# Optimization experiments

Hardware: AMD Instinct MI355X
Metric: run time of the kernel (lower is better)

Reference implementation:

```python
import jax, jax.numpy as jnp
import numpy as np

EMBED = 2048
HEADS = 16
KV_LEN = 4096
HEAD_DIM = EMBED // HEADS
LN_EPS = 1e-6


def _layernorm(x, scale, bias):
    m = jnp.mean(x, axis=-1, keepdims=True)
    v = jnp.var(x, axis=-1, keepdims=True)
    return (x - m) / jnp.sqrt(v + LN_EPS) * scale + bias


def setup_inputs() -> dict:
    key = jax.random.key(0)
    ks = jax.random.split(key, 12)
    d = EMBED
    s = 1.0 / np.sqrt(d)

    def W(k):
        return jax.random.normal(k, (d, d), jnp.float32) * s

    return {
        "x": jax.random.normal(ks[0], (d,), jnp.float32),
        "cache1": jax.random.normal(ks[1], (KV_LEN, HEADS, HEAD_DIM), jnp.float32),
        "cache2": jax.random.normal(ks[2], (KV_LEN, HEADS, HEAD_DIM), jnp.float32),
        "Wv": W(ks[3]), "bv": jnp.zeros((d,), jnp.float32),
        "Wq": W(ks[4]), "bq": jnp.zeros((d,), jnp.float32),
        "Wk": W(ks[5]), "bk": jnp.zeros((d,), jnp.float32),
        "Wo": W(ks[6]), "bo": jnp.zeros((d,), jnp.float32),
        "W1": W(ks[7]), "b1": jnp.zeros((d,), jnp.float32),
        "W2": W(ks[8]), "b2": jnp.zeros((d,), jnp.float32),
        "ln1_s": jnp.ones((d,), jnp.float32), "ln1_b": jnp.zeros((d,), jnp.float32),
        "ln2_s": jnp.ones((d,), jnp.float32), "ln2_b": jnp.zeros((d,), jnp.float32),
    }


def reference(x, cache1, cache2, Wv, bv, Wq, bq, Wk, bk, Wo, bo,
              W1, b1, W2, b2, ln1_s, ln1_b, ln2_s, ln2_b):
    H, hd = HEADS, HEAD_DIM
    # QKV projections for the single query token
    v_i = (x @ Wv + bv).reshape(1, H, hd)
    q_i = (x @ Wq + bq).reshape(H, hd)
    k_i = (x @ Wk + bk).reshape(1, H, hd)
    # roll caches: drop oldest, append newest
    v = jnp.concatenate((cache1[1:], v_i), axis=0)  # [K, H, hd]
    k = jnp.concatenate((cache2[1:], k_i), axis=0)
    # valid positions: any nonzero value in the v cache slot
    mask = jnp.any(v != 0, axis=(1, 2))  # [K]
    att = jnp.einsum('hd,khd->hk', q_i, k) / jnp.sqrt(jnp.float32(hd))
    att = jnp.where(mask, att, -jnp.inf)
    att = jax.nn.softmax(att, axis=-1)
    values = jnp.einsum('hk,khd->hd', att, v).reshape(EMBED)
    out = values @ Wo + bo
    # residual + LN, FFN (dropout deterministic -> no-op), residual + LN
    x1 = _layernorm(x + out, ln1_s, ln1_b)
    h = jax.nn.relu(x1 @ W1 + b1) @ W2 + b2
    x2 = _layernorm(x1 + h, ln2_s, ln2_b)
    return (x2, v, k)
```

## Files before the change

### kernel.cpp

```cpp
#include <hip/hip_runtime.h>
#include <hip/hip_bf16.h>
#include <stdint.h>

#define D    2048
#define H    16
#define HD   128
#define KV   4096
#define NCH  64
#define RPC  (D / NCH)
#define AVCH 64
#define AVR  (KV / AVCH)
#define RSQRT_HD 0.08838834764831845f

typedef __attribute__((ext_vector_type(4))) float floatx4;


__global__ void k_matvec_part(const float* __restrict__ W0,
                              const float* __restrict__ W1p,
                              const float* __restrict__ W2p,
                              const float* __restrict__ xin,
                              float* __restrict__ part) {
    const float* W = (blockIdx.y == 0) ? W0 : (blockIdx.y == 1 ? W1p : W2p);
    int c0 = threadIdx.x * 4;
    int r0 = blockIdx.x * RPC;
    floatx4 a0 = {0.f, 0.f, 0.f, 0.f};
    floatx4 a1 = {0.f, 0.f, 0.f, 0.f};
    for (int r = r0; r < r0 + RPC; ++r) {
        float xv = xin[r];
        floatx4 w0 = *reinterpret_cast<const floatx4*>(W + (size_t)r * D + c0);
        floatx4 w1 = *reinterpret_cast<const floatx4*>(W + (size_t)r * D + c0 + 1024);
        a0 += xv * w0;
        a1 += xv * w1;
    }
    float* p = part + ((size_t)blockIdx.y * NCH + blockIdx.x) * D;
    *reinterpret_cast<floatx4*>(p + c0) = a0;
    *reinterpret_cast<floatx4*>(p + c0 + 1024) = a1;
}

__global__ void k_qkv_reduce(const float* __restrict__ part,
                             const float* __restrict__ bq,
                             const float* __restrict__ bk,
                             const float* __restrict__ bv,
                             float* __restrict__ q, float* __restrict__ kn,
                             float* __restrict__ vn) {
    int t = blockIdx.x * 256 + threadIdx.x;
    int m = t >> 11;
    int col = t & (D - 1);
    float s = 0.f;
    const float* p = part + (size_t)m * NCH * D + col;
    for (int c = 0; c < NCH; ++c) s += p[(size_t)c * D];
    if (m == 0)      q[col]  = s + bq[col];
    else if (m == 1) kn[col] = s + bk[col];
    else             vn[col] = s + bv[col];
}

__global__ void k_roll_logits(const float* __restrict__ cache1,
                              const float* __restrict__ cache2,
                              const float* __restrict__ q,
                              const float* __restrict__ kn,
                              const float* __restrict__ vn,
                              float* __restrict__ outv,
                              float* __restrict__ outk,
                              float* __restrict__ att) {
    int wave = threadIdx.x >> 6;
    int lane = threadIdx.x & 63;
    int kk = blockIdx.x * 4 + wave;
    float pc[8];
    bool nz = false;

    if (kk < KV - 1) {
        const float* vsrc = cache1 + (size_t)(kk + 1) * D;
        const float* ksrc = cache2 + (size_t)(kk + 1) * D;
        float* vdst = outv + (size_t)kk * D;
        float* kdst = outk + (size_t)kk * D;
#pragma unroll
        for (int c = 0; c < 8; ++c) {
            int e = c * 256 + lane * 4;
            floatx4 v4 = *reinterpret_cast<const floatx4*>(vsrc + e);
            *reinterpret_cast<floatx4*>(vdst + e) = v4;
            nz = nz | (v4[0] != 0.f) | (v4[1] != 0.f) | (v4[2] != 0.f) | (v4[3] != 0.f);
            floatx4 k4 = *reinterpret_cast<const floatx4*>(ksrc + e);
            *reinterpret_cast<floatx4*>(kdst + e) = k4;
            floatx4 q4 = *reinterpret_cast<const floatx4*>(q + e);
            pc[c] = q4[0]*k4[0] + q4[1]*k4[1] + q4[2]*k4[2] + q4[3]*k4[3];
        }
    } else {
        float* vdst = outv + (size_t)kk * D;
        float* kdst = outk + (size_t)kk * D;
#pragma unroll
        for (int c = 0; c < 8; ++c) {
            int e = c * 256 + lane * 4;
            floatx4 v4, k4;
#pragma unroll
            for (int j = 0; j < 4; ++j) {
                v4[j] = vn[e + j];
                k4[j] = kn[e + j];
            }
            *reinterpret_cast<floatx4*>(vdst + e) = v4;
            *reinterpret_cast<floatx4*>(kdst + e) = k4;
            nz = nz | (v4[0] != 0.f) | (v4[1] != 0.f) | (v4[2] != 0.f) | (v4[3] != 0.f);
            floatx4 q4 = *reinterpret_cast<const floatx4*>(q + e);
            pc[c] = q4[0]*k4[0] + q4[1]*k4[1] + q4[2]*k4[2] + q4[3]*k4[3];
        }
    }

    unsigned long long bal = __ballot(nz ? 1 : 0);
    bool anynz = (bal != 0ULL);

#pragma unroll
    for (int c = 0; c < 8; ++c) {
        float v = pc[c];
        v += __shfl_xor(v, 1);
        v += __shfl_xor(v, 2);
        v += __shfl_xor(v, 4);
        v += __shfl_xor(v, 8);
        v += __shfl_xor(v, 16);
        pc[c] = v;
    }
    if ((lane & 31) == 0) {
        int hi = lane >> 5;
#pragma unroll
        for (int c = 0; c < 8; ++c) {
            int h = c * 2 + hi;
            att[(size_t)h * KV + kk] = anynz ? pc[c] * RSQRT_HD : -INFINITY;
        }
    }
}

__global__ void k_softmax(float* __restrict__ att) {
    __shared__ float sred[4];
    int h = blockIdx.x;
    float* a = att + (size_t)h * KV;
    int t = threadIdx.x;
    float v[16];
    float m = -INFINITY;
#pragma unroll
    for (int i = 0; i < 16; ++i) {
        v[i] = a[i * 256 + t];
        m = fmaxf(m, v[i]);
    }
    for (int s = 32; s >= 1; s >>= 1) m = fmaxf(m, __shfl_xor(m, s));
    if ((t & 63) == 0) sred[t >> 6] = m;
    __syncthreads();
    m = fmaxf(fmaxf(sred[0], sred[1]), fmaxf(sred[2], sred[3]));
    __syncthreads();
    float sum = 0.f;
#pragma unroll
    for (int i = 0; i < 16; ++i) {
        v[i] = __expf(v[i] - m);
        sum += v[i];
    }
    for (int s = 32; s >= 1; s >>= 1) sum += __shfl_xor(sum, s);
    if ((t & 63) == 0) sred[t >> 6] = sum;
    __syncthreads();
    sum = sred[0] + sred[1] + sred[2] + sred[3];
    float inv = 1.0f / sum;
#pragma unroll
    for (int i = 0; i < 16; ++i) a[i * 256 + t] = v[i] * inv;
}

__global__ void k_av_part(const float* __restrict__ outv,
                          const float* __restrict__ att,
                          float* __restrict__ pav) {
    int h = blockIdx.y;
    int c = blockIdx.x;
    int lane = threadIdx.x;
    int dg = (lane & 31) * 4;
    int ks = lane >> 5;
    floatx4 acc = {0.f, 0.f, 0.f, 0.f};
    int kk0 = c * AVR;
    for (int i = 0; i < AVR / 2; ++i) {
        int kk = kk0 + i * 2 + ks;
        float a = att[(size_t)h * KV + kk];
        floatx4 v4 = *reinterpret_cast<const floatx4*>(outv + (size_t)kk * D + h * HD + dg);
        acc += a * v4;
    }
#pragma unroll
    for (int j = 0; j < 4; ++j) acc[j] += __shfl_xor(acc[j], 32);
    if (lane < 32) {
        *reinterpret_cast<floatx4*>(pav + (size_t)c * D + h * HD + dg) = acc;
    }
}

__global__ void k_av_reduce(const float* __restrict__ pav, float* __restrict__ values) {
    int e = blockIdx.x * 256 + threadIdx.x;
    float s = 0.f;
    for (int c = 0; c < AVCH; ++c) s += pav[(size_t)c * D + e];
    values[e] = s;
}

__global__ void k_mv_reduce(const float* __restrict__ part,
                            const float* __restrict__ bias,
                            float* __restrict__ out, int relu) {
    int col = blockIdx.x * 256 + threadIdx.x;
    float s = 0.f;
    for (int c = 0; c < NCH; ++c) s += part[(size_t)c * D + col];
    s += bias[col];
    if (relu) s = fmaxf(s, 0.0f);
    out[col] = s;
}

__global__ void k_ln(const float* __restrict__ a, const float* __restrict__ b,
                     const float* __restrict__ sc, const float* __restrict__ bi,
                     float* __restrict__ out) {
    __shared__ float sred[4];
    int t = threadIdx.x;
    float loc[8];
    float s = 0.f;
#pragma unroll
    for (int i = 0; i < 8; ++i) {
        int e = i * 256 + t;
        float v = a[e] + b[e];
        loc[i] = v;
        s += v;
    }
    for (int m = 32; m >= 1; m >>= 1) s += __shfl_xor(s, m);
    if ((t & 63) == 0) sred[t >> 6] = s;
    __syncthreads();
    float mean = (sred[0] + sred[1] + sred[2] + sred[3]) * (1.0f / D);
    __syncthreads();
    float vs = 0.f;
#pragma unroll
    for (int i = 0; i < 8; ++i) {
        float d = loc[i] - mean;
        vs += d * d;
    }
    for (int m = 32; m >= 1; m >>= 1) vs += __shfl_xor(vs, m);
    if ((t & 63) == 0) sred[t >> 6] = vs;
    __syncthreads();
    float var = (sred[0] + sred[1] + sred[2] + sred[3]) * (1.0f / D);
    float inv = 1.0f / sqrtf(var + 1e-6f);
#pragma unroll
    for (int i = 0; i < 8; ++i) {
        int e = i * 256 + t;
        out[e] = (loc[i] - mean) * inv * sc[e] + bi[e];
    }
}

extern "C" void kernel_launch(void* const* d_in, const int* in_sizes, int n_in,
                              void* d_out, int out_size, void* d_ws, size_t ws_size,
                              hipStream_t stream) {
    const float* x      = (const float*)d_in[0];
    const float* cache1 = (const float*)d_in[1];
    const float* cache2 = (const float*)d_in[2];
    const float* Wv     = (const float*)d_in[3];
    const float* bv     = (const float*)d_in[4];
    const float* Wq     = (const float*)d_in[5];
    const float* bq     = (const float*)d_in[6];
    const float* Wk     = (const float*)d_in[7];
    const float* bk     = (const float*)d_in[8];
    const float* Wo     = (const float*)d_in[9];
    const float* bo     = (const float*)d_in[10];
    const float* W1     = (const float*)d_in[11];
    const float* b1     = (const float*)d_in[12];
    const float* W2     = (const float*)d_in[13];
    const float* b2     = (const float*)d_in[14];
    const float* l1s    = (const float*)d_in[15];
    const float* l1b    = (const float*)d_in[16];
    const float* l2s    = (const float*)d_in[17];
    const float* l2b    = (const float*)d_in[18];

    float* out   = (float*)d_out;
    float* outx2 = out;
    float* outv  = out + D;
    float* outk  = out + D + (size_t)KV * D;

    float* w      = (float*)d_ws;
    float* q      = w + 2048;
    float* kn     = w + 4096;
    float* vn     = w + 6144;
    float* att    = w + 8192;
    float* values = w + 73728;
    float* aout   = w + 75776;
    float* x1     = w + 77824;
    float* h1     = w + 79872;
    float* h2     = w + 81920;
    float* part   = w + 83968;
    float* pav    = w + 477184;

    k_matvec_part<<<dim3(NCH, 3), 256, 0, stream>>>(Wq, Wk, Wv, x, part);
    k_qkv_reduce<<<24, 256, 0, stream>>>(part, bq, bk, bv, q, kn, vn);
    k_roll_logits<<<KV / 4, 256, 0, stream>>>(cache1, cache2, q, kn, vn, outv, outk, att);
    k_softmax<<<H, 256, 0, stream>>>(att);
    k_av_part<<<dim3(AVCH, H), 64, 0, stream>>>(outv, att, pav);
    k_av_reduce<<<8, 256, 0, stream>>>(pav, values);
    k_matvec_part<<<dim3(NCH, 1), 256, 0, stream>>>(Wo, Wo, Wo, values, part);
    k_mv_reduce<<<8, 256, 0, stream>>>(part, bo, aout, 0);
    k_ln<<<1, 256, 0, stream>>>(x, aout, l1s, l1b, x1);
    k_matvec_part<<<dim3(NCH, 1), 256, 0, stream>>>(W1, W1, W1, x1, part);
    k_mv_reduce<<<8, 256, 0, stream>>>(part, b1, h1, 1);
    k_matvec_part<<<dim3(NCH, 1), 256, 0, stream>>>(W2, W2, W2, h1, part);
    k_mv_reduce<<<8, 256, 0, stream>>>(part, b2, h2, 0);
    k_ln<<<1, 256, 0, stream>>>(x1, h2, l2s, l2b, outx2);
}
```

Measured before the change: 281.5 us.

## Replace split-K partial buffers and reduce kernels with atomic accumulation and fused biases

Matvec and attention-value kernels now accumulate straight into zeroed outputs with float atomics, so the separate partial-sum reduce kernels and their scratch traffic go away. Biases and the ReLU are folded into the consumers (roll_logits, layernorm, the next matvec's input load), and a memset zeroes the accumulators up front. The matvec also loads 16 rows of weights at a time for more memory-level parallelism. This cuts the kernel launch count, at the cost of atomic contention and nondeterministic summation order.

After: 292.4 us. +3.9%, slower.

```diff
diff --git a/kernel.cpp b/kernel.cpp
--- a/kernel.cpp
+++ b/kernel.cpp
@@ -6,59 +6,46 @@
 #define H    16
 #define HD   128
 #define KV   4096
-#define NCH  64
-#define RPC  (D / NCH)
-#define AVCH 64
-#define AVR  (KV / AVCH)
 #define RSQRT_HD 0.08838834764831845f
 
 typedef __attribute__((ext_vector_type(4))) float floatx4;
 
 
-__global__ void k_matvec_part(const float* __restrict__ W0,
-                              const float* __restrict__ W1p,
-                              const float* __restrict__ W2p,
-                              const float* __restrict__ xin,
-                              float* __restrict__ part) {
-    const float* W = (blockIdx.y == 0) ? W0 : (blockIdx.y == 1 ? W1p : W2p);
+__global__ void k_matvec(const float* __restrict__ Wa, const float* __restrict__ Wb,
+                         const float* __restrict__ Wc, const float* __restrict__ xin,
+                         const float* __restrict__ prebias,
+                         float* __restrict__ dst) {
+    const float* W = (blockIdx.y == 0) ? Wa : (blockIdx.y == 1 ? Wb : Wc);
+    float* d = dst + (size_t)blockIdx.y * D;
     int c0 = threadIdx.x * 4;
-    int r0 = blockIdx.x * RPC;
-    floatx4 a0 = {0.f, 0.f, 0.f, 0.f};
-    floatx4 a1 = {0.f, 0.f, 0.f, 0.f};
-    for (int r = r0; r < r0 + RPC; ++r) {
-        float xv = xin[r];
-        floatx4 w0 = *reinterpret_cast<const floatx4*>(W + (size_t)r * D + c0);
-        floatx4 w1 = *reinterpret_cast<const floatx4*>(W + (size_t)r * D + c0 + 1024);
-        a0 += xv * w0;
-        a1 += xv * w1;
-    }
-    float* p = part + ((size_t)blockIdx.y * NCH + blockIdx.x) * D;
-    *reinterpret_cast<floatx4*>(p + c0) = a0;
-    *reinterpret_cast<floatx4*>(p + c0 + 1024) = a1;
-}
-
-__global__ void k_qkv_reduce(const float* __restrict__ part,
-                             const float* __restrict__ bq,
-                             const float* __restrict__ bk,
-                             const float* __restrict__ bv,
-                             float* __restrict__ q, float* __restrict__ kn,
-                             float* __restrict__ vn) {
-    int t = blockIdx.x * 256 + threadIdx.x;
-    int m = t >> 11;
-    int col = t & (D - 1);
-    float s = 0.f;
-    const float* p = part + (size_t)m * NCH * D + col;
-    for (int c = 0; c < NCH; ++c) s += p[(size_t)c * D];
-    if (m == 0)      q[col]  = s + bq[col];
-    else if (m == 1) kn[col] = s + bk[col];
-    else             vn[col] = s + bv[col];
+    int r0 = blockIdx.x * 32;
+    floatx4 acc = {0.f, 0.f, 0.f, 0.f};
+    for (int rb = 0; rb < 2; ++rb) {
+        const float* Wp = W + (size_t)(r0 + rb * 16) * D + c0;
+        floatx4 w[16];
+#pragma unroll
+        for (int i = 0; i < 16; ++i)
+            w[i] = *reinterpret_cast<const floatx4*>(Wp + (size_t)i * D);
+#pragma unroll
+        for (int i = 0; i < 16; ++i) {
+            int r = r0 + rb * 16 + i;
+            float t = xin[r];
+            if (prebias) t = fmaxf(t + prebias[r], 0.f);
+            acc += t * w[i];
+        }
+    }
+    atomicAdd(&d[c0 + 0], acc[0]);
+    atomicAdd(&d[c0 + 1], acc[1]);
+    atomicAdd(&d[c0 + 2], acc[2]);
+    atomicAdd(&d[c0 + 3], acc[3]);
 }
 
 __global__ void k_roll_logits(const float* __restrict__ cache1,
                               const float* __restrict__ cache2,
-                              const float* __restrict__ q,
-                              const float* __restrict__ kn,
-                              const float* __restrict__ vn,
+                              const float* __restrict__ qs,
+                              const float* __restrict__ bq,
+                              const float* __restrict__ bk,
+                              const float* __restrict__ bv,
                               float* __restrict__ outv,
                               float* __restrict__ outk,
                               float* __restrict__ att) {
@@ -67,39 +54,43 @@
     int kk = blockIdx.x * 4 + wave;
     float pc[8];
     bool nz = false;
+    float* vdst = outv + (size_t)kk * D;
+    float* kdst = outk + (size_t)kk * D;
 
     if (kk < KV - 1) {
         const float* vsrc = cache1 + (size_t)(kk + 1) * D;
         const float* ksrc = cache2 + (size_t)(kk + 1) * D;
-        float* vdst = outv + (size_t)kk * D;
-        float* kdst = outk + (size_t)kk * D;
+        floatx4 v[8], k[8];
+#pragma unroll
+        for (int c = 0; c < 8; ++c)
+            v[c] = *reinterpret_cast<const floatx4*>(vsrc + c * 256 + lane * 4);
+#pragma unroll
+        for (int c = 0; c < 8; ++c)
+            k[c] = *reinterpret_cast<const floatx4*>(ksrc + c * 256 + lane * 4);
 #pragma unroll
         for (int c = 0; c < 8; ++c) {
             int e = c * 256 + lane * 4;
-            floatx4 v4 = *reinterpret_cast<const floatx4*>(vsrc + e);
-            *reinterpret_cast<floatx4*>(vdst + e) = v4;
-            nz = nz | (v4[0] != 0.f) | (v4[1] != 0.f) | (v4[2] != 0.f) | (v4[3] != 0.f);
-            floatx4 k4 = *reinterpret_cast<const floatx4*>(ksrc + e);
-            *reinterpret_cast<floatx4*>(kdst + e) = k4;
-            floatx4 q4 = *reinterpret_cast<const floatx4*>(q + e);
-            pc[c] = q4[0]*k4[0] + q4[1]*k4[1] + q4[2]*k4[2] + q4[3]*k4[3];
+            *reinterpret_cast<floatx4*>(vdst + e) = v[c];
+            *reinterpret_cast<floatx4*>(kdst + e) = k[c];
+            nz = nz | (v[c][0] != 0.f) | (v[c][1] != 0.f) | (v[c][2] != 0.f) | (v[c][3] != 0.f);
+            floatx4 q4 = *reinterpret_cast<const floatx4*>(qs + e);
+            floatx4 b4 = *reinterpret_cast<const floatx4*>(bq + e);
+            q4 += b4;
+            pc[c] = q4[0]*k[c][0] + q4[1]*k[c][1] + q4[2]*k[c][2] + q4[3]*k[c][3];
         }
     } else {
-        float* vdst = outv + (size_t)kk * D;
-        float* kdst = outk + (size_t)kk * D;
 #pragma unroll
         for (int c = 0; c < 8; ++c) {
             int e = c * 256 + lane * 4;
-            floatx4 v4, k4;
-#pragma unroll
-            for (int j = 0; j < 4; ++j) {
-                v4[j] = vn[e + j];
-                k4[j] = kn[e + j];
-            }
+            floatx4 v4 = *reinterpret_cast<const floatx4*>(qs + 2 * D + e);
+            floatx4 k4 = *reinterpret_cast<const floatx4*>(qs + D + e);
+            v4 += *reinterpret_cast<const floatx4*>(bv + e);
+            k4 += *reinterpret_cast<const floatx4*>(bk + e);
             *reinterpret_cast<floatx4*>(vdst + e) = v4;
             *reinterpret_cast<floatx4*>(kdst + e) = k4;
             nz = nz | (v4[0] != 0.f) | (v4[1] != 0.f) | (v4[2] != 0.f) | (v4[3] != 0.f);
-            floatx4 q4 = *reinterpret_cast<const floatx4*>(q + e);
+            floatx4 q4 = *reinterpret_cast<const floatx4*>(qs + e);
+            q4 += *reinterpret_cast<const floatx4*>(bq + e);
             pc[c] = q4[0]*k4[0] + q4[1]*k4[1] + q4[2]*k4[2] + q4[3]*k4[3];
         }
     }
@@ -159,17 +150,18 @@
     for (int i = 0; i < 16; ++i) a[i * 256 + t] = v[i] * inv;
 }
 
-__global__ void k_av_part(const float* __restrict__ outv,
-                          const float* __restrict__ att,
-                          float* __restrict__ pav) {
+__global__ void k_av(const float* __restrict__ outv,
+                     const float* __restrict__ att,
+                     float* __restrict__ values) {
     int h = blockIdx.y;
     int c = blockIdx.x;
     int lane = threadIdx.x;
     int dg = (lane & 31) * 4;
     int ks = lane >> 5;
     floatx4 acc = {0.f, 0.f, 0.f, 0.f};
-    int kk0 = c * AVR;
-    for (int i = 0; i < AVR / 2; ++i) {
+    int kk0 = c * 64;
+#pragma unroll 8
+    for (int i = 0; i < 32; ++i) {
         int kk = kk0 + i * 2 + ks;
         float a = att[(size_t)h * KV + kk];
         floatx4 v4 = *reinterpret_cast<const floatx4*>(outv + (size_t)kk * D + h * HD + dg);
@@ -178,29 +170,16 @@
 #pragma unroll
     for (int j = 0; j < 4; ++j) acc[j] += __shfl_xor(acc[j], 32);
     if (lane < 32) {
-        *reinterpret_cast<floatx4*>(pav + (size_t)c * D + h * HD + dg) = acc;
-    }
-}
-
-__global__ void k_av_reduce(const float* __restrict__ pav, float* __restrict__ values) {
-    int e = blockIdx.x * 256 + threadIdx.x;
-    float s = 0.f;
-    for (int c = 0; c < AVCH; ++c) s += pav[(size_t)c * D + e];
-    values[e] = s;
-}
-
-__global__ void k_mv_reduce(const float* __restrict__ part,
-                            const float* __restrict__ bias,
-                            float* __restrict__ out, int relu) {
-    int col = blockIdx.x * 256 + threadIdx.x;
-    float s = 0.f;
-    for (int c = 0; c < NCH; ++c) s += part[(size_t)c * D + col];
-    s += bias[col];
-    if (relu) s = fmaxf(s, 0.0f);
-    out[col] = s;
+        float* p = values + h * HD + dg;
+        atomicAdd(&p[0], acc[0]);
+        atomicAdd(&p[1], acc[1]);
+        atomicAdd(&p[2], acc[2]);
+        atomicAdd(&p[3], acc[3]);
+    }
 }
 
 __global__ void k_ln(const float* __restrict__ a, const float* __restrict__ b,
+                     const float* __restrict__ bb,
                      const float* __restrict__ sc, const float* __restrict__ bi,
                      float* __restrict__ out) {
     __shared__ float sred[4];
@@ -210,7 +189,7 @@
 #pragma unroll
     for (int i = 0; i < 8; ++i) {
         int e = i * 256 + t;
-        float v = a[e] + b[e];
+        float v = a[e] + b[e] + bb[e];
         loc[i] = v;
         s += v;
     }
@@ -266,30 +245,23 @@
     float* outk  = out + D + (size_t)KV * D;
 
     float* w      = (float*)d_ws;
-    float* q      = w + 2048;
-    float* kn     = w + 4096;
-    float* vn     = w + 6144;
-    float* att    = w + 8192;
-    float* values = w + 73728;
-    float* aout   = w + 75776;
-    float* x1     = w + 77824;
-    float* h1     = w + 79872;
-    float* h2     = w + 81920;
-    float* part   = w + 83968;
-    float* pav    = w + 477184;
-
-    k_matvec_part<<<dim3(NCH, 3), 256, 0, stream>>>(Wq, Wk, Wv, x, part);
-    k_qkv_reduce<<<24, 256, 0, stream>>>(part, bq, bk, bv, q, kn, vn);
-    k_roll_logits<<<KV / 4, 256, 0, stream>>>(cache1, cache2, q, kn, vn, outv, outk, att);
+    float* qs     = w + 0;
+    float* values = w + 6144;
+    float* aout   = w + 8192;
+    float* h1     = w + 10240;
+    float* h2     = w + 12288;
+    float* x1     = w + 14336;
+    float* att    = w + 16384;
+
+    hipMemsetAsync(w, 0, 14336 * sizeof(float), stream);
+
+    k_matvec<<<dim3(64, 3), 512, 0, stream>>>(Wq, Wk, Wv, x, nullptr, qs);
+    k_roll_logits<<<KV / 4, 256, 0, stream>>>(cache1, cache2, qs, bq, bk, bv, outv, outk, att);
     k_softmax<<<H, 256, 0, stream>>>(att);
-    k_av_part<<<dim3(AVCH, H), 64, 0, stream>>>(outv, att, pav);
-    k_av_reduce<<<8, 256, 0, stream>>>(pav, values);
-    k_matvec_part<<<dim3(NCH, 1), 256, 0, stream>>>(Wo, Wo, Wo, values, part);
-    k_mv_reduce<<<8, 256, 0, stream>>>(part, bo, aout, 0);
-    k_ln<<<1, 256, 0, stream>>>(x, aout, l1s, l1b, x1);
-    k_matvec_part<<<dim3(NCH, 1), 256, 0, stream>>>(W1, W1, W1, x1, part);
-    k_mv_reduce<<<8, 256, 0, stream>>>(part, b1, h1, 1);
-    k_matvec_part<<<dim3(NCH, 1), 256, 0, stream>>>(W2, W2, W2, h1, part);
-    k_mv_reduce<<<8, 256, 0, stream>>>(part, b2, h2, 0);
-    k_ln<<<1, 256, 0, stream>>>(x1, h2, l2s, l2b, outx2);
-}
+    k_av<<<dim3(64, H), 64, 0, stream>>>(outv, att, values);
+    k_matvec<<<dim3(64, 1), 512, 0, stream>>>(Wo, Wo, Wo, values, nullptr, aout);
+    k_ln<<<1, 256, 0, stream>>>(x, aout, bo, l1s, l1b, x1);
+    k_matvec<<<dim3(64, 1), 512, 0, stream>>>(W1, W1, W1, x1, nullptr, h1);
+    k_matvec<<<dim3(64, 1), 512, 0, stream>>>(W2, W2, W2, h1, b1, h2);
+    k_ln<<<1, 256, 0, stream>>>(x1, h2, b2, l2s, l2b, outx2);
+}
```
